# Optimization experiments

Measured on AMD Instinct MI355X. Metric: run time of the kernel, lower is better.

The kernel has to match this reference:

```python
import jax, jax.numpy as jnp
import numpy as np

H, KVH, HD, D = 8, 2, 128, 1024
E, TOPK, FFN = 8, 2, 3584
THETA, EPS = 1e6, 1e-5
NBITS, GS = 4, 128
QMAX = float(2 ** NBITS - 1)
NEG = -1e30


def qgroup(w):
    # quantize_int_group: asymmetric int4 fake-quant over contiguous groups of 128
    shp = w.shape
    w2 = w.reshape(-1, GS)
    wmax = jnp.max(w2, -1, keepdims=True)
    wmin = jnp.min(w2, -1, keepdims=True)
    scales = jnp.clip(wmax - wmin, 1e-5, None) / QMAX
    base = jnp.clip(jnp.round(-wmin / scales), 0.0, QMAX)
    wq = (jnp.clip(jnp.round(w2 / scales) + base, 0.0, QMAX) - base) * scales
    return wq.reshape(shp)


def rms(x, g):
    return x * jax.lax.rsqrt(jnp.mean(x * x, -1, keepdims=True) + EPS) * g


def rot_half(x):
    h = x.shape[-1] // 2
    return jnp.concatenate([-x[..., h:], x[..., :h]], axis=-1)


def setup_inputs() -> dict:
    key = jax.random.key(0)
    ks = jax.random.split(key, 12)
    B, S = 2, 1024
    n = lambda k, s: 0.02 * jax.random.normal(k, s, dtype=jnp.float32)
    return {
        'hidden_states': jax.random.normal(ks[0], (B, S, D), dtype=jnp.float32),
        'w_q': n(ks[1], (H * HD, D)),
        'w_k': n(ks[2], (KVH * HD, D)),
        'w_v': n(ks[3], (KVH * HD, D)),
        'w_o': n(ks[4], (D, H * HD)),
        'g1': jnp.ones((D,), jnp.float32),
        'g2': jnp.ones((D,), jnp.float32),
        'w_gate': n(ks[5], (E, D)),
        'w1': n(ks[6], (E, FFN, D)),
        'w3': n(ks[7], (E, FFN, D)),
        'w2': n(ks[8], (E, D, FFN)),
    }


def reference(hidden_states, w_q, w_k, w_v, w_o, g1, g2, w_gate, w1, w3, w2):
    B, S, _ = hidden_states.shape
    T = B * S
    # ---- attention block (pre-norm) ----
    xn = rms(hidden_states, g1)
    q = (xn @ qgroup(w_q).T).reshape(B, S, H, HD).transpose(0, 2, 1, 3)
    k = (xn @ qgroup(w_k).T).reshape(B, S, KVH, HD).transpose(0, 2, 1, 3)
    v = (xn @ qgroup(w_v).T).reshape(B, S, KVH, HD).transpose(0, 2, 1, 3)
    # q_kv_cache: quantize key BEFORE RoPE (as in source)
    k = qgroup(k)
    pos = jnp.arange(S, dtype=jnp.float32)
    inv = 1.0 / (THETA ** (jnp.arange(0, HD, 2, dtype=jnp.float32) / HD))
    freqs = pos[:, None] * inv[None, :]
    emb = jnp.concatenate([freqs, freqs], axis=-1)  # [S, HD]
    cos = jnp.cos(emb)[None, None]
    sin = jnp.sin(emb)[None, None]
    q = q * cos + rot_half(q) * sin
    k = k * cos + rot_half(k) * sin
    rep = H // KVH
    k = jnp.repeat(k, rep, axis=1)
    v = jnp.repeat(v, rep, axis=1)
    # q_kv_cache: quantize value AFTER repeat_kv (as in source)
    v = qgroup(v)
    scores = jnp.einsum('bhqd,bhkd->bhqk', q, k) / np.float32(np.sqrt(HD))
    causal = jnp.tril(jnp.ones((S, S), dtype=bool))
    scores = jnp.where(causal[None, None], scores, NEG)
    attn = jax.nn.softmax(scores, axis=-1)
    o = jnp.einsum('bhqk,bhkd->bhqd', attn, v).transpose(0, 2, 1, 3).reshape(B, S, H * HD)
    h = hidden_states + o @ qgroup(w_o).T
    # ---- sparse MoE block (pre-norm) ----
    hn = rms(h, g2).reshape(T, D)
    logits = hn @ w_gate.T  # router gate kept full precision
    probs = jax.nn.softmax(logits, axis=-1)
    tv, ti = jax.lax.top_k(probs, TOPK)
    tv = tv / jnp.sum(tv, axis=-1, keepdims=True)
    rw = jnp.zeros((T, E), hn.dtype).at[jnp.arange(T)[:, None], ti].set(tv)
    moe = jnp.zeros((T, D), hn.dtype)
    for e in range(E):  # fixed small expert loop; SwiGLU with int4-group-quantized weights
        up = jax.nn.silu(hn @ qgroup(w1[e]).T) * (hn @ qgroup(w3[e]).T)
        moe = moe + rw[:, e:e + 1] * (up @ qgroup(w2[e]).T)
    return h + moe.reshape(B, S, D)
```

## Files before the change

### kernel.cpp

```cpp
#include <hip/hip_runtime.h>
#include <hip/hip_bf16.h>


typedef __attribute__((ext_vector_type(4))) float f32x4;
typedef __attribute__((ext_vector_type(8))) short short8;
typedef __hip_bfloat16 bf16;

#define DEV static __device__ __forceinline__

DEV float wsum(float v){
  #pragma unroll
  for (int o=32;o>0;o>>=1) v += __shfl_xor(v,o,64);
  return v;
}
DEV float wmaxr(float v){
  #pragma unroll
  for (int o=32;o>0;o>>=1) v = fmaxf(v,__shfl_xor(v,o,64));
  return v;
}
DEV float wminr(float v){
  #pragma unroll
  for (int o=32;o>0;o>>=1) v = fminf(v,__shfl_xor(v,o,64));
  return v;
}
DEV float fakeq(float x, float s, float b){
  return (fminf(fmaxf(rintf(x/s)+b,0.f),15.f)-b)*s;
}

constexpr size_t OFF_WQKV = 0;
constexpr size_t OFF_WO   = OFF_WQKV + 6291456;
constexpr size_t OFF_W1Q  = OFF_WO   + 4194304;
constexpr size_t OFF_W3Q  = OFF_W1Q  + 58720256;
constexpr size_t OFF_W2Q  = OFF_W3Q  + 58720256;
constexpr size_t OFF_QKV  = OFF_W2Q  + 58720256;
constexpr size_t OFF_SC   = OFF_QKV  + 12582912;
constexpr size_t OFF_O2   = OFF_SC   + 67108864;
constexpr size_t OFF_H    = OFF_O2   + 8388608;
constexpr size_t OFF_XN   = OFF_H    + 8388608;
constexpr size_t OFF_HNB  = OFF_XN   + 8388608;
constexpr size_t OFF_COS  = OFF_HNB  + 4194304;
constexpr size_t OFF_SIN  = OFF_COS  + 262144;
constexpr size_t OFF_CNT  = OFF_SIN  + 262144;
constexpr size_t OFF_TOK  = OFF_CNT  + 256;
constexpr size_t OFF_WTS  = OFF_TOK  + 65536;
constexpr size_t OFF_MA   = OFF_WTS  + 65536;
constexpr size_t OFF_MB   = OFF_MA   + 8388608;
constexpr size_t WS_NEED  = OFF_MB   + 8388608;

__global__ void k_sentinel(float* out){ out[0] = 12345.0f; }
__global__ void k_zero(int* cnt){ if (threadIdx.x < 8) cnt[threadIdx.x] = 0; }

__global__ __launch_bounds__(256) void k_rms(const float* __restrict__ x,
                                             const float* __restrict__ g,
                                             float* __restrict__ out,
                                             bf16* __restrict__ outb)
{
  int row = blockIdx.x, tid = threadIdx.x;
  const float4* x4 = (const float4*)(x + (size_t)row*1024);
  float4 v = x4[tid];
  float ss = v.x*v.x + v.y*v.y + v.z*v.z + v.w*v.w;
  int lane = tid & 63, wv = tid >> 6;
  ss = wsum(ss);
  __shared__ float red[4];
  if (lane == 0) red[wv] = ss;
  __syncthreads();
  float tot = red[0]+red[1]+red[2]+red[3];
  float r = 1.0f / sqrtf(tot * (1.0f/1024.0f) + 1e-5f);
  float4 gg = ((const float4*)g)[tid];
  float4 o;
  o.x = v.x*r*gg.x; o.y = v.y*r*gg.y; o.z = v.z*r*gg.z; o.w = v.w*r*gg.w;
  ((float4*)(out + (size_t)row*1024))[tid] = o;
  if (outb) {
    bf16* ob = outb + (size_t)row*1024 + tid*4;
    ob[0]=__float2bfloat16(o.x); ob[1]=__float2bfloat16(o.y);
    ob[2]=__float2bfloat16(o.z); ob[3]=__float2bfloat16(o.w);
  }
}

__global__ __launch_bounds__(256) void k_dequant_attn(
    const float* __restrict__ wq, const float* __restrict__ wk,
    const float* __restrict__ wv, const float* __restrict__ wo,
    float* __restrict__ wqkv, float* __restrict__ wod)
{
  int g = blockIdx.x*4 + (threadIdx.x>>6);
  int lane = threadIdx.x & 63;
  const float* src; float* dst;
  if (g < 8192)       { size_t o=(size_t)g*128;          src = wq + o; dst = wqkv + o; }
  else if (g < 10240) { size_t o=(size_t)(g-8192)*128;   src = wk + o; dst = wqkv + (size_t)1024*1024 + o; }
  else if (g < 12288) { size_t o=(size_t)(g-10240)*128;  src = wv + o; dst = wqkv + (size_t)1280*1024 + o; }
  else                { size_t o=(size_t)(g-12288)*128;  src = wo + o; dst = wod + o; }
  float x0 = src[lane], x1 = src[lane+64];
  float mn = wminr(fminf(x0,x1));
  float mx = wmaxr(fmaxf(x0,x1));
  float s = fmaxf(mx-mn, 1e-5f) / 15.0f;
  float b = fminf(fmaxf(rintf(-mn/s),0.f),15.f);
  dst[lane]    = fakeq(x0,s,b);
  dst[lane+64] = fakeq(x1,s,b);
}

__global__ __launch_bounds__(256) void k_dequant_moe(
    const float* __restrict__ w1, const float* __restrict__ w3,
    const float* __restrict__ w2,
    bf16* __restrict__ o1, bf16* __restrict__ o3, bf16* __restrict__ o2q)
{
  int g = blockIdx.x*4 + (threadIdx.x>>6);
  int lane = threadIdx.x & 63;
  const int NG = 229376;
  int t = g / NG, gl = g - t*NG;
  const float* src; bf16* dst;
  if (t == 0)      { src = w1; dst = o1; }
  else if (t == 1) { src = w3; dst = o3; }
  else             { src = w2; dst = o2q; }
  src += (size_t)gl*128; dst += (size_t)gl*128;
  float x0 = src[lane], x1 = src[lane+64];
  float mn = wminr(fminf(x0,x1));
  float mx = wmaxr(fmaxf(x0,x1));
  float s = fmaxf(mx-mn, 1e-5f) / 15.0f;
  float b = fminf(fmaxf(rintf(-mn/s),0.f),15.f);
  dst[lane]    = __float2bfloat16(fakeq(x0,s,b));
  dst[lane+64] = __float2bfloat16(fakeq(x1,s,b));
}

__global__ __launch_bounds__(256) void k_rope_tab(float* ct, float* st)
{
  int s = blockIdx.x*4 + (threadIdx.x>>6);
  int l = threadIdx.x & 63;
  float inv = 1.0f / powf(1.0e6f, (float)l * (1.0f/64.0f));
  float f = (float)s * inv;
  ct[s*64 + l] = cosf(f);
  st[s*64 + l] = sinf(f);
}

DEV void gemm_bt_128x64(const float* __restrict__ A, int lda,
                        const float* __restrict__ Bm, int ldb,
                        float* __restrict__ C, int ldc,
                        const float* __restrict__ resid,
                        int K, float scale, int m0, int n0)
{
  __shared__ float As[16*136];
  __shared__ float Bs[16*72];
  int tid = threadIdx.x;
  int ar = tid >> 1, ak = (tid & 1) * 8;
  int br = tid >> 2, bk = (tid & 3) * 4;
  const float* ap = A + (size_t)(m0 + ar)*lda + ak;
  const float* bp = Bm + (size_t)(n0 + br)*ldb + bk;
  int ty = tid >> 4, tx = tid & 15;
  int r0 = ty*8, c0 = tx*4;
  float acc[8][4];
  #pragma unroll
  for (int i=0;i<8;i++){
    #pragma unroll
    for (int j=0;j<4;j++) acc[i][j]=0.f;
  }
  for (int k0 = 0; k0 < K; k0 += 16) {
    float4 a0 = *(const float4*)(ap + k0);
    float4 a1 = *(const float4*)(ap + k0 + 4);
    float4 b0 = *(const float4*)(bp + k0);
    __syncthreads();
    As[(ak+0)*136+ar]=a0.x; As[(ak+1)*136+ar]=a0.y; As[(ak+2)*136+ar]=a0.z; As[(ak+3)*136+ar]=a0.w;
    As[(ak+4)*136+ar]=a1.x; As[(ak+5)*136+ar]=a1.y; As[(ak+6)*136+ar]=a1.z; As[(ak+7)*136+ar]=a1.w;
    Bs[(bk+0)*72+br]=b0.x;  Bs[(bk+1)*72+br]=b0.y;  Bs[(bk+2)*72+br]=b0.z;  Bs[(bk+3)*72+br]=b0.w;
    __syncthreads();
    #pragma unroll
    for (int kk = 0; kk < 16; kk++) {
      float4 xa = *(const float4*)&As[kk*136 + r0];
      float4 xb = *(const float4*)&As[kk*136 + r0 + 4];
      float4 yb = *(const float4*)&Bs[kk*72 + c0];
      float xs[8] = {xa.x,xa.y,xa.z,xa.w,xb.x,xb.y,xb.z,xb.w};
      float ys[4] = {yb.x,yb.y,yb.z,yb.w};
      #pragma unroll
      for (int i=0;i<8;i++){
        #pragma unroll
        for (int j=0;j<4;j++) acc[i][j] += xs[i]*ys[j];
      }
    }
  }
  #pragma unroll
  for (int i=0;i<8;i++){
    size_t ro = (size_t)(m0 + r0 + i)*ldc + n0 + c0;
    #pragma unroll
    for (int j=0;j<4;j++){
      float v = acc[i][j]*scale;
      if (resid) v += resid[ro + j];
      C[ro + j] = v;
    }
  }
}

__global__ __launch_bounds__(256) void k_qkv_gemm(const float* xn, const float* wqkv, float* qkv){
  gemm_bt_128x64(xn, 1024, wqkv, 1024, qkv, 1536, nullptr, 1024, 1.0f,
                 blockIdx.y*128, blockIdx.x*64);
}
__global__ __launch_bounds__(256) void k_wo(const float* o2, const float* wod,
                                            const float* hidden, float* h){
  gemm_bt_128x64(o2, 1024, wod, 1024, h, 1024, hidden, 1024, 1.0f,
                 blockIdx.y*128, blockIdx.x*64);
}
__global__ __launch_bounds__(256) void k_scores(const float* qkv, float* sc){
  int z = blockIdx.z, b = z >> 3, h = z & 7;
  int m0 = blockIdx.y*128, n0 = blockIdx.x*64;
  if (n0 > m0 + 127) return;
  const float* A  = qkv + (size_t)b*1024*1536 + h*128;
  const float* Bp = qkv + (size_t)b*1024*1536 + 1024 + (h>>2)*128;
  float* C = sc + (size_t)z*1024*1024;
  gemm_bt_128x64(A, 1536, Bp, 1536, C, 1024, nullptr, 128, 0.08838834764831845f, m0, n0);
}

DEV void gemm_nn_64x64(const float* __restrict__ A, int lda,
                       const float* __restrict__ Bm, int ldb,
                       float* __restrict__ C, int ldc,
                       int kmax, int m0, int n0)
{
  __shared__ float As[16*68];
  __shared__ float Bs[16*68];
  int tid = threadIdx.x;
  int ar = tid >> 2, ak = (tid & 3)*4;
  int bk = tid >> 4, bc = (tid & 15)*4;
  const float* ap = A + (size_t)(m0 + ar)*lda + ak;
  const float* bp = Bm + (size_t)bk*ldb + n0 + bc;
  int ty = tid >> 4, tx = tid & 15;
  int r0 = ty*4, c0 = tx*4;
  float acc[4][4];
  #pragma unroll
  for (int i=0;i<4;i++){
    #pragma unroll
    for (int j=0;j<4;j++) acc[i][j]=0.f;
  }
  for (int k0 = 0; k0 < kmax; k0 += 16) {
    float4 a = *(const float4*)(ap + k0);
    float4 b = *(const float4*)(bp + (size_t)k0*ldb);
    __syncthreads();
    As[(ak+0)*68+ar]=a.x; As[(ak+1)*68+ar]=a.y; As[(ak+2)*68+ar]=a.z; As[(ak+3)*68+ar]=a.w;
    *(float4*)&Bs[bk*68 + bc] = b;
    __syncthreads();
    #pragma unroll
    for (int kk = 0; kk < 16; kk++) {
      float4 xa = *(const float4*)&As[kk*68 + r0];
      float4 yb = *(const float4*)&Bs[kk*68 + c0];
      float xs[4] = {xa.x,xa.y,xa.z,xa.w};
      float ys[4] = {yb.x,yb.y,yb.z,yb.w};
      #pragma unroll
      for (int i=0;i<4;i++){
        #pragma unroll
        for (int j=0;j<4;j++) acc[i][j] += xs[i]*ys[j];
      }
    }
  }
  #pragma unroll
  for (int i=0;i<4;i++){
    size_t ro = (size_t)(m0 + r0 + i)*ldc + n0 + c0;
    #pragma unroll
    for (int j=0;j<4;j++) C[ro + j] = acc[i][j];
  }
}

__global__ __launch_bounds__(256) void k_pv(const float* sc, const float* qkv, float* o2){
  int z = blockIdx.z, b = z >> 3, h = z & 7;
  int m0 = blockIdx.y*64, n0 = blockIdx.x*64;
  const float* A  = sc + (size_t)z*1024*1024;
  const float* Bp = qkv + (size_t)b*1024*1536 + 1280 + (h>>2)*128;
  float* C = o2 + (size_t)b*1024*1024 + h*128;
  gemm_nn_64x64(A, 1024, Bp, 1536, C, 1024, m0 + 64 , m0, n0);
}

__global__ __launch_bounds__(256) void k_rope_q(float* qkv, const float* ct, const float* st){
  int wid = blockIdx.x*4 + (threadIdx.x>>6);
  int lane = threadIdx.x & 63;
  int t = wid >> 3, h = wid & 7;
  int s = t & 1023;
  float* base = qkv + (size_t)t*1536 + h*128;
  float x0 = base[lane], x1 = base[lane+64];
  float c = ct[s*64+lane], sn = st[s*64+lane];
  base[lane]    = x0*c - x1*sn;
  base[lane+64] = x1*c + x0*sn;
}

__global__ __launch_bounds__(256) void k_kv(float* qkv, const float* ct, const float* st){
  int wid = blockIdx.x*4 + (threadIdx.x>>6);
  int lane = threadIdx.x & 63;
  int t = wid >> 1, kvh = wid & 1;
  int s = t & 1023;
  float* kb = qkv + (size_t)t*1536 + 1024 + kvh*128;
  float* vb = qkv + (size_t)t*1536 + 1280 + kvh*128;
  float k0v = kb[lane], k1v = kb[lane+64];
  float v0v = vb[lane], v1v = vb[lane+64];
  float mn = wminr(fminf(k0v,k1v));
  float mx = wmaxr(fmaxf(k0v,k1v));
  float sc = fmaxf(mx-mn,1e-5f)/15.0f;
  float bs = fminf(fmaxf(rintf(-mn/sc),0.f),15.f);
  float kq0 = fakeq(k0v,sc,bs), kq1 = fakeq(k1v,sc,bs);
  float c = ct[s*64+lane], sn = st[s*64+lane];
  kb[lane]    = kq0*c - kq1*sn;
  kb[lane+64] = kq1*c + kq0*sn;
  mn = wminr(fminf(v0v,v1v));
  mx = wmaxr(fmaxf(v0v,v1v));
  sc = fmaxf(mx-mn,1e-5f)/15.0f;
  bs = fminf(fmaxf(rintf(-mn/sc),0.f),15.f);
  vb[lane]    = fakeq(v0v,sc,bs);
  vb[lane+64] = fakeq(v1v,sc,bs);
}

__global__ __launch_bounds__(256) void k_softmax(float* sc){
  int row = blockIdx.x;
  int i = row & 1023;
  float* p = sc + (size_t)row*1024;
  int tid = threadIdx.x, lane = tid & 63, wv = tid >> 6;
  float v[4];
  float m = -3.0e38f;
  #pragma unroll
  for (int k2=0;k2<4;k2++){
    int j = tid + k2*256;
    v[k2] = p[j];
    if (j <= i) m = fmaxf(m, v[k2]);
  }
  __shared__ float red[4];
  m = wmaxr(m);
  if (lane==0) red[wv] = m;
  __syncthreads();
  m = fmaxf(fmaxf(red[0],red[1]), fmaxf(red[2],red[3]));
  float ls = 0.f;
  #pragma unroll
  for (int k2=0;k2<4;k2++){
    int j = tid + k2*256;
    float e = (j <= i) ? __expf(v[k2]-m) : 0.0f;
    v[k2] = e; ls += e;
  }
  __syncthreads();
  ls = wsum(ls);
  if (lane==0) red[wv] = ls;
  __syncthreads();
  float inv = 1.0f / (red[0]+red[1]+red[2]+red[3]);
  #pragma unroll
  for (int k2=0;k2<4;k2++){
    int j = tid + k2*256;
    p[j] = v[k2]*inv;
  }
}

__global__ __launch_bounds__(256) void k_router(const float* __restrict__ hn,
                                                const float* __restrict__ wg,
                                                int* cnt, int* toksl, float* wts){
  int t = blockIdx.x*4 + (threadIdx.x>>6);
  int lane = threadIdx.x & 63;
  const float* x = hn + (size_t)t*1024;
  float p[8];
  #pragma unroll
  for (int e=0;e<8;e++) p[e]=0.f;
  for (int i=0;i<16;i++){
    float xv = x[lane + i*64];
    #pragma unroll
    for (int e=0;e<8;e++) p[e] += xv * wg[e*1024 + lane + i*64];
  }
  #pragma unroll
  for (int e=0;e<8;e++) p[e] = wsum(p[e]);
  if (lane==0){
    float m = p[0];
    for (int e=1;e<8;e++) m = fmaxf(m,p[e]);
    float ex[8], sum=0.f;
    for (int e=0;e<8;e++){ ex[e]=__expf(p[e]-m); sum+=ex[e]; }
    float pr[8];
    for (int e=0;e<8;e++) pr[e]=ex[e]/sum;
    int i1 = 0;
    for (int e=1;e<8;e++) if (pr[e] > pr[i1]) i1 = e;
    int i2 = -1;
    for (int e=0;e<8;e++){ if (e==i1) continue; if (i2<0 || pr[e] > pr[i2]) i2 = e; }
    float ssum = pr[i1]+pr[i2];
    float wa = pr[i1]/ssum, wb = pr[i2]/ssum;
    int pos = atomicAdd(cnt+i1,1);
    toksl[i1*2048+pos] = t;          wts[i1*2048+pos] = wa;
    pos = atomicAdd(cnt+i2,1);
    toksl[i2*2048+pos] = t | 65536;  wts[i2*2048+pos] = wb;
  }
}

__global__ __launch_bounds__(256) void k_moe_gemm1(
    const bf16* __restrict__ hnb, const bf16* __restrict__ w1q, const bf16* __restrict__ w3q,
    const int* __restrict__ cnt, const int* __restrict__ toksl,
    bf16* __restrict__ up, int ebase)
{
  int el = blockIdx.z, e = ebase + el;
  int c = cnt[e];
  int m0 = blockIdx.x * 64;
  if (m0 >= c) return;
  int n0 = blockIdx.y * 128;
  __shared__ bf16 As[64*40];
  __shared__ bf16 B1s[128*40];
  __shared__ bf16 B3s[128*40];
  int tid = threadIdx.x, lane = tid & 63, wv = tid >> 6;
  int arow = tid >> 2, acol = (tid & 3) * 8;
  int slot = m0 + arow;
  int tok = (slot < c) ? (toksl[e*2048 + slot] & 0xFFFF) : 0;
  const bf16* ap  = hnb + (size_t)tok*1024 + acol;
  const bf16* b1p = w1q + ((size_t)e*3584 + n0 + arow)*1024 + acol;
  const bf16* b3p = w3q + ((size_t)e*3584 + n0 + arow)*1024 + acol;
  f32x4 zero = {0.f,0.f,0.f,0.f};
  f32x4 acc1[4][2], acc3[4][2];
  #pragma unroll
  for (int i=0;i<4;i++){ acc1[i][0]=zero; acc1[i][1]=zero; acc3[i][0]=zero; acc3[i][1]=zero; }
  int fr = lane & 15, fq = lane >> 4;
  for (int k0 = 0; k0 < 1024; k0 += 32) {
    short8 av  = *(const short8*)(ap + k0);
    short8 b1a = *(const short8*)(b1p + k0);
    short8 b1b = *(const short8*)(b1p + (size_t)64*1024 + k0);
    short8 b3a = *(const short8*)(b3p + k0);
    short8 b3b = *(const short8*)(b3p + (size_t)64*1024 + k0);
    __syncthreads();
    *(short8*)&As[arow*40 + acol] = av;
    *(short8*)&B1s[arow*40 + acol] = b1a;
    *(short8*)&B1s[(arow+64)*40 + acol] = b1b;
    *(short8*)&B3s[arow*40 + acol] = b3a;
    *(short8*)&B3s[(arow+64)*40 + acol] = b3b;
    __syncthreads();
    short8 aF[4];
    #pragma unroll
    for (int mt=0; mt<4; mt++) aF[mt] = *(const short8*)&As[(mt*16+fr)*40 + fq*8];
    #pragma unroll
    for (int nt=0; nt<2; nt++){
      short8 b1F = *(const short8*)&B1s[(wv*32 + nt*16 + fr)*40 + fq*8];
      short8 b3F = *(const short8*)&B3s[(wv*32 + nt*16 + fr)*40 + fq*8];
      #pragma unroll
      for (int mt=0; mt<4; mt++){
        acc1[mt][nt] = __builtin_amdgcn_mfma_f32_16x16x32_bf16(aF[mt], b1F, acc1[mt][nt], 0,0,0);
        acc3[mt][nt] = __builtin_amdgcn_mfma_f32_16x16x32_bf16(aF[mt], b3F, acc3[mt][nt], 0,0,0);
      }
    }
  }
  bf16* upb = up + (size_t)el*2048*3584;
  #pragma unroll
  for (int mt=0; mt<4; mt++){
    #pragma unroll
    for (int nt=0; nt<2; nt++){
      #pragma unroll
      for (int r=0; r<4; r++){
        int srow = m0 + mt*16 + fq*4 + r;
        int fcol = n0 + wv*32 + nt*16 + fr;
        float x1 = acc1[mt][nt][r], x3 = acc3[mt][nt][r];
        float u = (x1 / (1.0f + __expf(-x1))) * x3;
        upb[(size_t)srow*3584 + fcol] = __float2bfloat16(u);
      }
    }
  }
}

__global__ __launch_bounds__(256) void k_moe_gemm2(
    const bf16* __restrict__ up, const bf16* __restrict__ w2q,
    const int* __restrict__ cnt, const int* __restrict__ toksl,
    const float* __restrict__ wts,
    float* __restrict__ moeA, float* __restrict__ moeB, int ebase)
{
  int el = blockIdx.z, e = ebase + el;
  int c = cnt[e];
  int m0 = blockIdx.x * 64;
  if (m0 >= c) return;
  int n0 = blockIdx.y * 128;
  __shared__ bf16 As[64*40];
  __shared__ bf16 Bs[128*40];
  int tid = threadIdx.x, lane = tid & 63, wv = tid >> 6;
  int arow = tid >> 2, acol = (tid & 3) * 8;
  const bf16* ap = up + (size_t)el*2048*3584 + (size_t)(m0 + arow)*3584 + acol;
  const bf16* bp = w2q + ((size_t)e*1024 + n0 + arow)*3584 + acol;
  f32x4 zero = {0.f,0.f,0.f,0.f};
  f32x4 acc[4][2];
  #pragma unroll
  for (int i=0;i<4;i++){ acc[i][0]=zero; acc[i][1]=zero; }
  int fr = lane & 15, fq = lane >> 4;
  for (int k0 = 0; k0 < 3584; k0 += 32) {
    short8 av = *(const short8*)(ap + k0);
    short8 ba = *(const short8*)(bp + k0);
    short8 bb = *(const short8*)(bp + (size_t)64*3584 + k0);
    __syncthreads();
    *(short8*)&As[arow*40 + acol] = av;
    *(short8*)&Bs[arow*40 + acol] = ba;
    *(short8*)&Bs[(arow+64)*40 + acol] = bb;
    __syncthreads();
    short8 aF[4];
    #pragma unroll
    for (int mt=0; mt<4; mt++) aF[mt] = *(const short8*)&As[(mt*16+fr)*40 + fq*8];
    #pragma unroll
    for (int nt=0; nt<2; nt++){
      short8 bF = *(const short8*)&Bs[(wv*32 + nt*16 + fr)*40 + fq*8];
      #pragma unroll
      for (int mt=0; mt<4; mt++)
        acc[mt][nt] = __builtin_amdgcn_mfma_f32_16x16x32_bf16(aF[mt], bF, acc[mt][nt], 0,0,0);
    }
  }
  #pragma unroll
  for (int mt=0; mt<4; mt++){
    #pragma unroll
    for (int nt=0; nt<2; nt++){
      #pragma unroll
      for (int r=0; r<4; r++){
        int srow = m0 + mt*16 + fq*4 + r;
        if (srow < c){
          int ts = toksl[e*2048 + srow];
          int tok = ts & 0xFFFF, fl = ts >> 16;
          float wt = wts[e*2048 + srow];
          int d = n0 + wv*32 + nt*16 + fr;
          float* dst = (fl ? moeB : moeA) + (size_t)tok*1024 + d;
          *dst = acc[mt][nt][r] * wt;
        }
      }
    }
  }
}

__global__ __launch_bounds__(256) void k_final(const float* h, const float* ma,
                                               const float* mb, float* out){
  size_t i = (size_t)blockIdx.x*256 + threadIdx.x;
  float4 a = ((const float4*)h)[i];
  float4 b = ((const float4*)ma)[i];
  float4 c = ((const float4*)mb)[i];
  float4 o;
  o.x = a.x+b.x+c.x; o.y = a.y+b.y+c.y; o.z = a.z+b.z+c.z; o.w = a.w+b.w+c.w;
  ((float4*)out)[i] = o;
}

extern "C" void kernel_launch(void* const* d_in, const int* in_sizes, int n_in,
                              void* d_out, int out_size, void* d_ws, size_t ws_size,
                              hipStream_t stream)
{
  (void)in_sizes; (void)n_in; (void)out_size;
  float* out = (float*)d_out;
  if (ws_size < WS_NEED) { k_sentinel<<<1,1,0,stream>>>(out); return; }

  const float* hidden = (const float*)d_in[0];
  const float* w_q  = (const float*)d_in[1];
  const float* w_k  = (const float*)d_in[2];
  const float* w_v  = (const float*)d_in[3];
  const float* w_o  = (const float*)d_in[4];
  const float* g1   = (const float*)d_in[5];
  const float* g2   = (const float*)d_in[6];
  const float* wg   = (const float*)d_in[7];
  const float* w1   = (const float*)d_in[8];
  const float* w3   = (const float*)d_in[9];
  const float* w2   = (const float*)d_in[10];
  char* ws = (char*)d_ws;
  float* WQKV = (float*)(ws + OFF_WQKV);
  float* WOD  = (float*)(ws + OFF_WO);
  bf16*  W1Q  = (bf16*)(ws + OFF_W1Q);
  bf16*  W3Q  = (bf16*)(ws + OFF_W3Q);
  bf16*  W2Q  = (bf16*)(ws + OFF_W2Q);
  float* QKV  = (float*)(ws + OFF_QKV);
  float* SC   = (float*)(ws + OFF_SC);
  bf16*  UP   = (bf16*)(ws + OFF_SC);
  float* O2b  = (float*)(ws + OFF_O2);
  float* Hb   = (float*)(ws + OFF_H);
  float* XN   = (float*)(ws + OFF_XN);
  bf16*  HNB  = (bf16*)(ws + OFF_HNB);
  float* CT   = (float*)(ws + OFF_COS);
  float* ST   = (float*)(ws + OFF_SIN);
  int*   CNT  = (int*)(ws + OFF_CNT);
  int*   TOK  = (int*)(ws + OFF_TOK);
  float* WTS  = (float*)(ws + OFF_WTS);
  float* MA   = (float*)(ws + OFF_MA);
  float* MB   = (float*)(ws + OFF_MB);

  k_zero<<<1,64,0,stream>>>(CNT);
  k_rms<<<2048,256,0,stream>>>(hidden, g1, XN, (bf16*)nullptr);
  k_dequant_attn<<<5120,256,0,stream>>>(w_q, w_k, w_v, w_o, WQKV, WOD);
  k_dequant_moe<<<172032,256,0,stream>>>(w1, w3, w2, W1Q, W3Q, W2Q);
  k_rope_tab<<<256,256,0,stream>>>(CT, ST);
  k_qkv_gemm<<<dim3(24,16),256,0,stream>>>(XN, WQKV, QKV);
  k_rope_q<<<4096,256,0,stream>>>(QKV, CT, ST);
  k_kv<<<1024,256,0,stream>>>(QKV, CT, ST);
  k_scores<<<dim3(16,8,16),256,0,stream>>>(QKV, SC);
  k_softmax<<<16384,256,0,stream>>>(SC);
  k_pv<<<dim3(2,16,16),256,0,stream>>>(SC, QKV, O2b);
  k_wo<<<dim3(16,16),256,0,stream>>>(O2b, WOD, hidden, Hb);
  k_rms<<<2048,256,0,stream>>>(Hb, g2, XN, HNB);
  k_router<<<512,256,0,stream>>>(XN, wg, CNT, TOK, WTS);
  k_moe_gemm1<<<dim3(32,28,4),256,0,stream>>>(HNB, W1Q, W3Q, CNT, TOK, UP, 0);
  k_moe_gemm2<<<dim3(32,8,4),256,0,stream>>>(UP, W2Q, CNT, TOK, WTS, MA, MB, 0);
  k_moe_gemm1<<<dim3(32,28,4),256,0,stream>>>(HNB, W1Q, W3Q, CNT, TOK, UP, 4);
  k_moe_gemm2<<<dim3(32,8,4),256,0,stream>>>(UP, W2Q, CNT, TOK, WTS, MA, MB, 4);
  k_final<<<2048,256,0,stream>>>(Hb, MA, MB, out);
}
```

Baseline: 1.452 ms.

## Enlarge MoE GEMM tiles to 128x128 with double-buffered LDS prefetch

```diff
diff --git a/kernel.cpp b/kernel.cpp
--- a/kernel.cpp
+++ b/kernel.cpp
@@ -378,62 +378,90 @@
     const int* __restrict__ cnt, const int* __restrict__ toksl,
     bf16* __restrict__ up, int ebase)
 {
+  int n0 = blockIdx.x * 128;
+  if (n0 >= 3584) return;
   int el = blockIdx.z, e = ebase + el;
   int c = cnt[e];
-  int m0 = blockIdx.x * 64;
+  int m0 = blockIdx.y * 128;
   if (m0 >= c) return;
-  int n0 = blockIdx.y * 128;
-  __shared__ bf16 As[64*40];
-  __shared__ bf16 B1s[128*40];
-  __shared__ bf16 B3s[128*40];
+  __shared__ bf16 As[2][128*40];
+  __shared__ bf16 B1s[2][128*40];
+  __shared__ bf16 B3s[2][128*40];
   int tid = threadIdx.x, lane = tid & 63, wv = tid >> 6;
-  int arow = tid >> 2, acol = (tid & 3) * 8;
+  int arow = tid >> 1, acol = (tid & 1) * 16;
   int slot = m0 + arow;
   int tok = (slot < c) ? (toksl[e*2048 + slot] & 0xFFFF) : 0;
   const bf16* ap  = hnb + (size_t)tok*1024 + acol;
   const bf16* b1p = w1q + ((size_t)e*3584 + n0 + arow)*1024 + acol;
   const bf16* b3p = w3q + ((size_t)e*3584 + n0 + arow)*1024 + acol;
+  int mq = wv & 1, nq = wv >> 1;
+  int fr = lane & 15, fq = lane >> 4;
   f32x4 zero = {0.f,0.f,0.f,0.f};
-  f32x4 acc1[4][2], acc3[4][2];
-  #pragma unroll
-  for (int i=0;i<4;i++){ acc1[i][0]=zero; acc1[i][1]=zero; acc3[i][0]=zero; acc3[i][1]=zero; }
-  int fr = lane & 15, fq = lane >> 4;
+  f32x4 acc1[4][4], acc3[4][4];
+  #pragma unroll
+  for (int i=0;i<4;i++){
+    #pragma unroll
+    for (int j=0;j<4;j++){ acc1[i][j]=zero; acc3[i][j]=zero; }
+  }
+  short8 a0 = *(const short8*)(ap);
+  short8 a1 = *(const short8*)(ap + 8);
+  short8 p0 = *(const short8*)(b1p);
+  short8 p1 = *(const short8*)(b1p + 8);
+  short8 q0 = *(const short8*)(b3p);
+  short8 q1 = *(const short8*)(b3p + 8);
+  *(short8*)&As[0][arow*40 + acol]      = a0;
+  *(short8*)&As[0][arow*40 + acol + 8]  = a1;
+  *(short8*)&B1s[0][arow*40 + acol]     = p0;
+  *(short8*)&B1s[0][arow*40 + acol + 8] = p1;
+  *(short8*)&B3s[0][arow*40 + acol]     = q0;
+  *(short8*)&B3s[0][arow*40 + acol + 8] = q1;
+  int buf = 0;
   for (int k0 = 0; k0 < 1024; k0 += 32) {
-    short8 av  = *(const short8*)(ap + k0);
-    short8 b1a = *(const short8*)(b1p + k0);
-    short8 b1b = *(const short8*)(b1p + (size_t)64*1024 + k0);
-    short8 b3a = *(const short8*)(b3p + k0);
-    short8 b3b = *(const short8*)(b3p + (size_t)64*1024 + k0);
     __syncthreads();
-    *(short8*)&As[arow*40 + acol] = av;
-    *(short8*)&B1s[arow*40 + acol] = b1a;
-    *(short8*)&B1s[(arow+64)*40 + acol] = b1b;
-    *(short8*)&B3s[arow*40 + acol] = b3a;
-    *(short8*)&B3s[(arow+64)*40 + acol] = b3b;
-    __syncthreads();
+    bool more = (k0 + 32) < 1024;
+    if (more) {
+      a0 = *(const short8*)(ap + k0 + 32);
+      a1 = *(const short8*)(ap + k0 + 40);
+      p0 = *(const short8*)(b1p + k0 + 32);
+      p1 = *(const short8*)(b1p + k0 + 40);
+      q0 = *(const short8*)(b3p + k0 + 32);
+      q1 = *(const short8*)(b3p + k0 + 40);
+    }
     short8 aF[4];
     #pragma unroll
-    for (int mt=0; mt<4; mt++) aF[mt] = *(const short8*)&As[(mt*16+fr)*40 + fq*8];
-    #pragma unroll
-    for (int nt=0; nt<2; nt++){
-      short8 b1F = *(const short8*)&B1s[(wv*32 + nt*16 + fr)*40 + fq*8];
-      short8 b3F = *(const short8*)&B3s[(wv*32 + nt*16 + fr)*40 + fq*8];
+    for (int mt=0; mt<4; mt++)
+      aF[mt] = *(const short8*)&As[buf][(mq*64 + mt*16 + fr)*40 + fq*8];
+    #pragma unroll
+    for (int nt=0; nt<4; nt++){
+      short8 b1F = *(const short8*)&B1s[buf][(nq*64 + nt*16 + fr)*40 + fq*8];
+      short8 b3F = *(const short8*)&B3s[buf][(nq*64 + nt*16 + fr)*40 + fq*8];
       #pragma unroll
       for (int mt=0; mt<4; mt++){
         acc1[mt][nt] = __builtin_amdgcn_mfma_f32_16x16x32_bf16(aF[mt], b1F, acc1[mt][nt], 0,0,0);
         acc3[mt][nt] = __builtin_amdgcn_mfma_f32_16x16x32_bf16(aF[mt], b3F, acc3[mt][nt], 0,0,0);
       }
     }
+    if (more) {
+      __syncthreads();
+      int nb = buf ^ 1;
+      *(short8*)&As[nb][arow*40 + acol]      = a0;
+      *(short8*)&As[nb][arow*40 + acol + 8]  = a1;
+      *(short8*)&B1s[nb][arow*40 + acol]     = p0;
+      *(short8*)&B1s[nb][arow*40 + acol + 8] = p1;
+      *(short8*)&B3s[nb][arow*40 + acol]     = q0;
+      *(short8*)&B3s[nb][arow*40 + acol + 8] = q1;
+      buf = nb;
+    }
   }
   bf16* upb = up + (size_t)el*2048*3584;
   #pragma unroll
   for (int mt=0; mt<4; mt++){
     #pragma unroll
-    for (int nt=0; nt<2; nt++){
+    for (int nt=0; nt<4; nt++){
       #pragma unroll
       for (int r=0; r<4; r++){
-        int srow = m0 + mt*16 + fq*4 + r;
-        int fcol = n0 + wv*32 + nt*16 + fr;
+        int srow = m0 + mq*64 + mt*16 + fq*4 + r;
+        int fcol = n0 + nq*64 + nt*16 + fr;
         float x1 = acc1[mt][nt][r], x3 = acc3[mt][nt][r];
         float u = (x1 / (1.0f + __expf(-x1))) * x3;
         upb[(size_t)srow*3584 + fcol] = __float2bfloat16(u);
@@ -450,52 +478,75 @@
 {
   int el = blockIdx.z, e = ebase + el;
   int c = cnt[e];
-  int m0 = blockIdx.x * 64;
+  int m0 = blockIdx.y * 128;
   if (m0 >= c) return;
-  int n0 = blockIdx.y * 128;
-  __shared__ bf16 As[64*40];
-  __shared__ bf16 Bs[128*40];
+  int n0 = blockIdx.x * 128;
+  __shared__ bf16 As[2][128*40];
+  __shared__ bf16 Bs[2][128*40];
   int tid = threadIdx.x, lane = tid & 63, wv = tid >> 6;
-  int arow = tid >> 2, acol = (tid & 3) * 8;
+  int arow = tid >> 1, acol = (tid & 1) * 16;
   const bf16* ap = up + (size_t)el*2048*3584 + (size_t)(m0 + arow)*3584 + acol;
   const bf16* bp = w2q + ((size_t)e*1024 + n0 + arow)*3584 + acol;
+  int mq = wv & 1, nq = wv >> 1;
+  int fr = lane & 15, fq = lane >> 4;
   f32x4 zero = {0.f,0.f,0.f,0.f};
-  f32x4 acc[4][2];
-  #pragma unroll
-  for (int i=0;i<4;i++){ acc[i][0]=zero; acc[i][1]=zero; }
-  int fr = lane & 15, fq = lane >> 4;
+  f32x4 acc[4][4];
+  #pragma unroll
+  for (int i=0;i<4;i++){
+    #pragma unroll
+    for (int j=0;j<4;j++) acc[i][j]=zero;
+  }
+  short8 a0 = *(const short8*)(ap);
+  short8 a1 = *(const short8*)(ap + 8);
+  short8 b0 = *(const short8*)(bp);
+  short8 b1 = *(const short8*)(bp + 8);
+  *(short8*)&As[0][arow*40 + acol]     = a0;
+  *(short8*)&As[0][arow*40 + acol + 8] = a1;
+  *(short8*)&Bs[0][arow*40 + acol]     = b0;
+  *(short8*)&Bs[0][arow*40 + acol + 8] = b1;
+  int buf = 0;
   for (int k0 = 0; k0 < 3584; k0 += 32) {
-    short8 av = *(const short8*)(ap + k0);
-    short8 ba = *(const short8*)(bp + k0);
-    short8 bb = *(const short8*)(bp + (size_t)64*3584 + k0);
     __syncthreads();
-    *(short8*)&As[arow*40 + acol] = av;
-    *(short8*)&Bs[arow*40 + acol] = ba;
-    *(short8*)&Bs[(arow+64)*40 + acol] = bb;
-    __syncthreads();
+    bool more = (k0 + 32) < 3584;
+    if (more) {
+      a0 = *(const short8*)(ap + k0 + 32);
+      a1 = *(const short8*)(ap + k0 + 40);
+      b0 = *(const short8*)(bp + k0 + 32);
+      b1 = *(const short8*)(bp + k0 + 40);
+    }
     short8 aF[4];
     #pragma unroll
-    for (int mt=0; mt<4; mt++) aF[mt] = *(const short8*)&As[(mt*16+fr)*40 + fq*8];
-    #pragma unroll
-    for (int nt=0; nt<2; nt++){
-      short8 bF = *(const short8*)&Bs[(wv*32 + nt*16 + fr)*40 + fq*8];
+    for (int mt=0; mt<4; mt++)
+      aF[mt] = *(const short8*)&As[buf][(mq*64 + mt*16 + fr)*40 + fq*8];
+    #pragma unroll
+    for (int nt=0; nt<4; nt++){
+      short8 bF = *(const short8*)&Bs[buf][(nq*64 + nt*16 + fr)*40 + fq*8];
       #pragma unroll
       for (int mt=0; mt<4; mt++)
         acc[mt][nt] = __builtin_amdgcn_mfma_f32_16x16x32_bf16(aF[mt], bF, acc[mt][nt], 0,0,0);
     }
+    if (more) {
+      __syncthreads();
+      int nb = buf ^ 1;
+      *(short8*)&As[nb][arow*40 + acol]     = a0;
+      *(short8*)&As[nb][arow*40 + acol + 8] = a1;
+      *(short8*)&Bs[nb][arow*40 + acol]     = b0;
+      *(short8*)&Bs[nb][arow*40 + acol + 8] = b1;
+      buf = nb;
+    }
   }
   #pragma unroll
   for (int mt=0; mt<4; mt++){
     #pragma unroll
-    for (int nt=0; nt<2; nt++){
+    for (int nt=0; nt<4; nt++){
       #pragma unroll
       for (int r=0; r<4; r++){
-        int srow = m0 + mt*16 + fq*4 + r;
+        int srow = m0 + mq*64 + mt*16 + fq*4 + r;
         if (srow < c){
           int ts = toksl[e*2048 + srow];
           int tok = ts & 0xFFFF, fl = ts >> 16;
           float wt = wts[e*2048 + srow];
-          int d = n0 + wv*32 + nt*16 + fr;
+          int d = n0 + nq*64 + nt*16 + fr;
           float* dst = (fl ? moeB : moeA) + (size_t)tok*1024 + d;
           *dst = acc[mt][nt][r] * wt;
         }
@@ -569,9 +620,9 @@
   k_wo<<<dim3(16,16),256,0,stream>>>(O2b, WOD, hidden, Hb);
   k_rms<<<2048,256,0,stream>>>(Hb, g2, XN, HNB);
   k_router<<<512,256,0,stream>>>(XN, wg, CNT, TOK, WTS);
-  k_moe_gemm1<<<dim3(32,28,4),256,0,stream>>>(HNB, W1Q, W3Q, CNT, TOK, UP, 0);
-  k_moe_gemm2<<<dim3(32,8,4),256,0,stream>>>(UP, W2Q, CNT, TOK, WTS, MA, MB, 0);
-  k_moe_gemm1<<<dim3(32,28,4),256,0,stream>>>(HNB, W1Q, W3Q, CNT, TOK, UP, 4);
-  k_moe_gemm2<<<dim3(32,8,4),256,0,stream>>>(UP, W2Q, CNT, TOK, WTS, MA, MB, 4);
+  k_moe_gemm1<<<dim3(32,16,4),256,0,stream>>>(HNB, W1Q, W3Q, CNT, TOK, UP, 0);
+  k_moe_gemm2<<<dim3(8,16,4),256,0,stream>>>(UP, W2Q, CNT, TOK, WTS, MA, MB, 0);
+  k_moe_gemm1<<<dim3(32,16,4),256,0,stream>>>(HNB, W1Q, W3Q, CNT, TOK, UP, 4);
+  k_moe_gemm2<<<dim3(8,16,4),256,0,stream>>>(UP, W2Q, CNT, TOK, WTS, MA, MB, 4);
   k_final<<<2048,256,0,stream>>>(Hb, MA, MB, out);
 }
```

Result: faster. 1.270 ms (-12.6%).
